# Optimization experiments

Hardware: AMD Instinct MI355X
Metric: run time of the kernel (lower is better)

## Reference

```python
import jax, jax.numpy as jnp
import numpy as np

B, C, H, W = 4, 64, 128, 128
O = 64
K, S, P, D = 3, 1, 1, 1
K2 = K * K
Ho = (H + 2 * P - D * (K - 1) - 1) // S + 1
Wo = (W + 2 * P - D * (K - 1) - 1) // S + 1


def setup_inputs() -> dict:
    key = jax.random.key(0)
    k1, k2, k3, k4, k5 = jax.random.split(key, 5)
    x = jax.random.normal(k1, (B, C, H, W), dtype=jnp.float32)
    fan = C * K2
    # offset conv: out_channels = 2*n_offsets*K*K = 18; small init so offsets are ~O(1) px
    offset_w = jax.random.normal(k2, (2 * K2, C, K, K), dtype=jnp.float32) * (0.1 / np.sqrt(fan))
    offset_b = jax.random.normal(k3, (2 * K2,), dtype=jnp.float32) * 0.01
    deform_w = jax.random.normal(k4, (O, C, K, K), dtype=jnp.float32) * (1.0 / np.sqrt(fan))
    deform_b = jax.random.normal(k5, (O,), dtype=jnp.float32) * 0.01
    return {"x": x, "offset_w": offset_w, "offset_b": offset_b,
            "deform_w": deform_w, "deform_b": deform_b}


def _conv2d(x, w, b):
    y = jax.lax.conv_general_dilated(
        x, w, window_strides=(S, S), padding=[(P, P), (P, P)],
        rhs_dilation=(D, D), dimension_numbers=("NCHW", "OIHW", "NCHW"))
    return y + b[None, :, None, None]


def _gather(flat, iy, ix, h, w):
    # flat: [B, C, H*W]; iy/ix: [B, K2, Ho, Wo] int32
    valid = (iy >= 0) & (iy < h) & (ix >= 0) & (ix < w)
    idx = jnp.clip(iy, 0, h - 1) * w + jnp.clip(ix, 0, w - 1)
    b = flat.shape[0]
    v = jax.vmap(lambda f, i: f[:, i])(flat, idx.reshape(b, -1))  # [B, C, K2*Ho*Wo]
    v = v.reshape(b, flat.shape[1], *idx.shape[1:])               # [B, C, K2, Ho, Wo]
    return v * valid[:, None].astype(flat.dtype)


def _deform_conv(x, offset, w, b):
    # offset: [B, 2*K2, Ho, Wo] laid out as (dy, dx) pairs per kernel tap (torchvision order)
    off = offset.reshape(B, K2, 2, Ho, Wo)
    dy, dx = off[:, :, 0], off[:, :, 1]                           # [B, K2, Ho, Wo]
    ky = (jnp.arange(K2) // K * D).astype(jnp.float32)
    kx = (jnp.arange(K2) % K * D).astype(jnp.float32)
    base_y = (jnp.arange(Ho) * S - P).astype(jnp.float32)
    base_x = (jnp.arange(Wo) * S - P).astype(jnp.float32)
    py = dy + base_y[None, None, :, None] + ky[None, :, None, None]
    px = dx + base_x[None, None, None, :] + kx[None, :, None, None]

    y0 = jnp.floor(py); x0 = jnp.floor(px)
    wy = py - y0; wx = px - x0
    y0i = y0.astype(jnp.int32); x0i = x0.astype(jnp.int32)
    flat = x.reshape(B, C, H * W)
    w00 = ((1 - wy) * (1 - wx))[:, None]
    w01 = ((1 - wy) * wx)[:, None]
    w10 = (wy * (1 - wx))[:, None]
    w11 = (wy * wx)[:, None]
    sampled = (_gather(flat, y0i, x0i, H, W) * w00
               + _gather(flat, y0i, x0i + 1, H, W) * w01
               + _gather(flat, y0i + 1, x0i, H, W) * w10
               + _gather(flat, y0i + 1, x0i + 1, H, W) * w11)  # [B, C, K2, Ho, Wo]
    out = jnp.einsum("bckhw,ock->bohw", sampled, w.reshape(O, C, K2))
    return out + b[None, :, None, None]


def reference(x, offset_w, offset_b, deform_w, deform_b):
    offset = _conv2d(x, offset_w, offset_b)
    return _deform_conv(x, offset, deform_w, deform_b)
```

## Files before the change

### kernel.cpp

```cpp
#include <hip/hip_runtime.h>

#define BB 4
#define CC 64
#define HH 128
#define WW 128
#define OO 64
#define HWs (HH*WW)
#define R9 9
#define XW 20

typedef _Float16 f16;
typedef _Float16 f16x8 __attribute__((ext_vector_type(8)));
typedef _Float16 f16x2 __attribute__((ext_vector_type(2)));
typedef float f32x4 __attribute__((ext_vector_type(4)));

__device__ __forceinline__ size_t xt_idx(int b, int y, int x) {
    return (((size_t)b * HH + y) * WW + x) * CC;
}

__global__ __launch_bounds__(256) void prep_all(const float* __restrict__ x,
                                                const float* __restrict__ offw,
                                                const float* __restrict__ dw,
                                                f16* __restrict__ xt,
                                                f16* __restrict__ wA_off,
                                                f16* __restrict__ wA_def) {
    const int bid = blockIdx.x;
    const int tid = threadIdx.x;
    if (bid < 512) {
        const int b = bid >> 7, y = bid & 127;
        const int px = tid & 127, half = tid >> 7;
        const float* src = x + (size_t)b * CC * HWs + (size_t)half * 32 * HWs + y * WW + px;
        f16* dst = xt + xt_idx(b, y, px) + half * 32;
        #pragma unroll
        for (int cg = 0; cg < 4; ++cg) {
            f16x8 v;
            #pragma unroll
            for (int j = 0; j < 8; ++j)
                v[j] = (f16)src[(size_t)(cg * 8 + j) * HWs];
            *(f16x8*)(dst + cg * 8) = v;
        }
    } else {
        const int t = (bid - 512) * 256 + tid;
        const int l = t & 63;
        const int idx = t >> 6;
        f16x8 v;
        if (idx < 36) {
            const int mt = idx & 1, ks = idx >> 1;
            const int o = mt * 16 + (l & 15);
            const int tap = ks >> 1, ky = tap / 3, kx = tap % 3;
            #pragma unroll
            for (int i = 0; i < 8; ++i) {
                const int c = (ks & 1) * 32 + (l >> 4) * 8 + i;
                v[i] = (o < 18) ? (f16)offw[((o * CC + c) * 3 + ky) * 3 + kx] : (f16)0.f;
            }
            *(f16x8*)(wA_off + (size_t)(idx * 64 + l) * 8) = v;
        } else if (idx < 108) {
            const int id2 = idx - 36;
            const int mt = id2 & 3, ks = (id2 >> 2) & 1, tap = id2 >> 3;
            const int o = mt * 16 + (l & 15);
            #pragma unroll
            for (int i = 0; i < 8; ++i) {
                const int c = ks * 32 + (l >> 4) * 8 + i;
                v[i] = (f16)dw[(size_t)(o * CC + c) * 9 + tap];
            }
            *(f16x8*)(wA_def + (size_t)(id2 * 64 + l) * 8) = v;
        }
    }
}

__device__ __forceinline__ f16x8 combine4(f16x8 p00, f16x8 p01, f16x8 p10, f16x8 p11,
                                          f16 h00, f16 h01, f16 h10, f16 h11) {
    const f16x8 W00 = {h00,h00,h00,h00,h00,h00,h00,h00};
    const f16x8 W01 = {h01,h01,h01,h01,h01,h01,h01,h01};
    const f16x8 W10 = {h10,h10,h10,h10,h10,h10,h10,h10};
    const f16x8 W11 = {h11,h11,h11,h11,h11,h11,h11,h11};
    return p00 * W00 + p01 * W01 + p10 * W10 + p11 * W11;
}

__global__ __launch_bounds__(256, 4) void deform_mfma(
    const f16* __restrict__ xt,
    const f16* __restrict__ wA_off,
    const float* __restrict__ offb,
    const f16* __restrict__ wA_def,
    const float* __restrict__ dbias,
    float* __restrict__ out)
{
    __shared__ __align__(16) char win[R9 * XW * 8 * 16];
    __shared__ float offs[18][64];

    const int tid = threadIdx.x;
    const int bid0 = blockIdx.x;
    const int bid = (bid0 & 7) * 128 + (bid0 >> 3);
    const int b  = bid >> 8;
    const int rg = (bid >> 3) & 31;
    const int pg = bid & 7;
    const int r0 = rg * 4, px0 = pg * 16;

    const int ri = tid >> 6, l = tid & 63;
    const int pxs = l & 15, cg = l >> 4;
    const int row = r0 + ri;
    const int gpx = px0 + pxs;
    const int slot = ri * 16 + pxs;

    #pragma unroll
    for (int it = 0; it < 6; ++it) {
        const int i = tid + it * 256;
        if (i < R9 * XW * 8) {
            const int s = i / (XW * 8), rem = i - s * (XW * 8);
            const int xw = rem >> 3, ch8 = rem & 7;
            const int gy = r0 - 2 + s, gx = px0 - 2 + xw;
            f16x8 v = {};
            if (gy >= 0 && gy < HH && gx >= 0 && gx < WW)
                v = *(const f16x8*)(xt + xt_idx(b, gy, gx) + ch8 * 8);
            *(f16x8*)(win + ((s * XW + xw) * 8 + (ch8 ^ ((xw + s) & 7))) * 16) = v;
        }
    }
    __syncthreads();

    {
        f32x4 oa0 = {0,0,0,0}, oa1 = {0,0,0,0};
        #pragma unroll
        for (int ks = 0; ks < 18; ++ks) {
            const int tap = ks >> 1, chalf = ks & 1;
            const int ky = tap / 3, kx = tap - ky * 3;
            const int s = ri + 1 + ky;
            const int xw = pxs + 1 + kx;
            const int ch8 = chalf * 4 + cg;
            const f16x8 bf = *(const f16x8*)(win + ((s * XW + xw) * 8 + (ch8 ^ ((xw + s) & 7))) * 16);
            const f16x8 a0 = *(const f16x8*)(wA_off + (size_t)((ks * 2 + 0) * 64 + l) * 8);
            const f16x8 a1 = *(const f16x8*)(wA_off + (size_t)((ks * 2 + 1) * 64 + l) * 8);
            oa0 = __builtin_amdgcn_mfma_f32_16x16x32_f16(a0, bf, oa0, 0, 0, 0);
            oa1 = __builtin_amdgcn_mfma_f32_16x16x32_f16(a1, bf, oa1, 0, 0, 0);
        }
        #pragma unroll
        for (int reg = 0; reg < 4; ++reg) {
            const int c0 = cg * 4 + reg;
            offs[c0][slot] = oa0[reg] + offb[c0];
            const int c1 = c0 + 16;
            if (c1 < 18) offs[c1][slot] = oa1[reg] + offb[c1];
        }
    }
    __syncthreads();

    int o00[9], o01[9], o10[9], o11[9];
    f16x2 hA[9], hB[9];
    unsigned okm = 0;
    #pragma unroll
    for (int t = 0; t < 9; ++t) {
        const int ky = t / 3, kx = t - ky * 3;
        const float dy = offs[2 * t][slot], dx = offs[2 * t + 1][slot];
        const float py  = (float)(row - 1 + ky) + dy;
        const float pxf = (float)(gpx - 1 + kx) + dx;
        const float y0f = floorf(py), x0f = floorf(pxf);
        const float wy = py - y0f, wx = pxf - x0f;
        const int y0 = (int)y0f, x0 = (int)x0f;
        const int y1 = y0 + 1, x1 = x0 + 1;
        const bool vy0 = (y0 >= 0) & (y0 < HH), vy1 = (y1 >= 0) & (y1 < HH);
        const bool vx0 = (x0 >= 0) & (x0 < WW), vx1 = (x1 >= 0) & (x1 < WW);
        hA[t][0] = (f16)((1.f - wy) * (1.f - wx) * (float)(vy0 & vx0));
        hA[t][1] = (f16)((1.f - wy) * wx         * (float)(vy0 & vx1));
        hB[t][0] = (f16)(wy * (1.f - wx)         * (float)(vy1 & vx0));
        hB[t][1] = (f16)(wy * wx                 * (float)(vy1 & vx1));
        const int cy0 = min(max(y0, 0), HH - 1), cy1 = min(max(y1, 0), HH - 1);
        const int cx0 = min(max(x0, 0), WW - 1), cx1 = min(max(x1, 0), WW - 1);
        const int s0 = cy0 - (r0 - 2), s1 = cy1 - (r0 - 2);
        const int u0 = cx0 - (px0 - 2), u1 = cx1 - (px0 - 2);
        const int ok = (s0 >= 0) & (s0 < R9) & (s1 >= 0) & (s1 < R9) &
                       (u0 >= 0) & (u0 < XW) & (u1 >= 0) & (u1 < XW);
        if (__all(ok)) okm |= (1u << t);
        const int s0c = min(max(s0, 0), R9 - 1), s1c = min(max(s1, 0), R9 - 1);
        const int u0c = min(max(u0, 0), XW - 1), u1c = min(max(u1, 0), XW - 1);
        o00[t] = ((s0c * XW + u0c) * 8 + (cg ^ ((u0c + s0c) & 7))) * 16;
        o01[t] = ((s0c * XW + u1c) * 8 + (cg ^ ((u1c + s0c) & 7))) * 16;
        o10[t] = ((s1c * XW + u0c) * 8 + (cg ^ ((u0c + s1c) & 7))) * 16;
        o11[t] = ((s1c * XW + u1c) * 8 + (cg ^ ((u1c + s1c) & 7))) * 16;
    }

    f32x4 acc0 = {0,0,0,0}, acc1 = {0,0,0,0}, acc2 = {0,0,0,0}, acc3 = {0,0,0,0};
    const f16* wbase = wA_def + (size_t)l * 8;

    if (okm == 0x1FFu) {
        #pragma unroll
        for (int j = 0; j < 18; ++j) {
            const int t = j >> 1, fl = (j & 1) << 6;
            const f16x8 p00 = *(const f16x8*)(win + (o00[t] ^ fl));
            const f16x8 p01 = *(const f16x8*)(win + (o01[t] ^ fl));
            const f16x8 p10 = *(const f16x8*)(win + (o10[t] ^ fl));
            const f16x8 p11 = *(const f16x8*)(win + (o11[t] ^ fl));
            const f16x8 bf = combine4(p00, p01, p10, p11,
                                      hA[t][0], hA[t][1], hB[t][0], hB[t][1]);
            const f16* wa = wbase + (size_t)j * 2048;
            acc0 = __builtin_amdgcn_mfma_f32_16x16x32_f16(*(const f16x8*)(wa + 0 * 512), bf, acc0, 0, 0, 0);
            acc1 = __builtin_amdgcn_mfma_f32_16x16x32_f16(*(const f16x8*)(wa + 1 * 512), bf, acc1, 0, 0, 0);
            acc2 = __builtin_amdgcn_mfma_f32_16x16x32_f16(*(const f16x8*)(wa + 2 * 512), bf, acc2, 0, 0, 0);
            acc3 = __builtin_amdgcn_mfma_f32_16x16x32_f16(*(const f16x8*)(wa + 3 * 512), bf, acc3, 0, 0, 0);
        }
    } else {
        #pragma unroll
        for (int t = 0; t < 9; ++t) {
            #pragma unroll
            for (int cpass = 0; cpass < 2; ++cpass) {
                const int flip = cpass << 6;
                f16x8 bf;
                if ((okm >> t) & 1) {
                    const f16x8 p00 = *(const f16x8*)(win + (o00[t] ^ flip));
                    const f16x8 p01 = *(const f16x8*)(win + (o01[t] ^ flip));
                    const f16x8 p10 = *(const f16x8*)(win + (o10[t] ^ flip));
                    const f16x8 p11 = *(const f16x8*)(win + (o11[t] ^ flip));
                    bf = combine4(p00, p01, p10, p11,
                                  hA[t][0], hA[t][1], hB[t][0], hB[t][1]);
                } else {
                    const int ky = t / 3, kx = t - ky * 3;
                    const float dy = offs[2 * t][slot], dx = offs[2 * t + 1][slot];
                    const float py  = (float)(row - 1 + ky) + dy;
                    const float pxf = (float)(gpx - 1 + kx) + dx;
                    const int y0 = (int)floorf(py), x0 = (int)floorf(pxf);
                    const int cy0 = min(max(y0, 0), HH - 1), cy1 = min(max(y0 + 1, 0), HH - 1);
                    const int cx0 = min(max(x0, 0), WW - 1), cx1 = min(max(x0 + 1, 0), WW - 1);
                    const int ch8 = cpass * 4 + cg;
                    const f16x8 p00 = *(const f16x8*)(xt + xt_idx(b, cy0, cx0) + ch8 * 8);
                    const f16x8 p01 = *(const f16x8*)(xt + xt_idx(b, cy0, cx1) + ch8 * 8);
                    const f16x8 p10 = *(const f16x8*)(xt + xt_idx(b, cy1, cx0) + ch8 * 8);
                    const f16x8 p11 = *(const f16x8*)(xt + xt_idx(b, cy1, cx1) + ch8 * 8);
                    bf = combine4(p00, p01, p10, p11,
                                  hA[t][0], hA[t][1], hB[t][0], hB[t][1]);
                }
                const f16* wa = wbase + (size_t)(t * 2 + cpass) * 2048;
                acc0 = __builtin_amdgcn_mfma_f32_16x16x32_f16(*(const f16x8*)(wa + 0 * 512), bf, acc0, 0, 0, 0);
                acc1 = __builtin_amdgcn_mfma_f32_16x16x32_f16(*(const f16x8*)(wa + 1 * 512), bf, acc1, 0, 0, 0);
                acc2 = __builtin_amdgcn_mfma_f32_16x16x32_f16(*(const f16x8*)(wa + 2 * 512), bf, acc2, 0, 0, 0);
                acc3 = __builtin_amdgcn_mfma_f32_16x16x32_f16(*(const f16x8*)(wa + 3 * 512), bf, acc3, 0, 0, 0);
            }
        }
    }

    #pragma unroll
    for (int mt = 0; mt < 4; ++mt) {
        const f32x4 a = (mt == 0) ? acc0 : (mt == 1) ? acc1 : (mt == 2) ? acc2 : acc3;
        #pragma unroll
        for (int reg = 0; reg < 4; ++reg) {
            const int o = mt * 16 + cg * 4 + reg;
            out[(((size_t)b * OO + o) * HH + row) * WW + gpx] = a[reg] + dbias[o];
        }
    }
}

extern "C" void kernel_launch(void* const* d_in, const int* in_sizes, int n_in,
                              void* d_out, int out_size, void* d_ws, size_t ws_size,
                              hipStream_t stream) {
    const float* x     = (const float*)d_in[0];
    const float* offw  = (const float*)d_in[1];
    const float* offb  = (const float*)d_in[2];
    const float* dw    = (const float*)d_in[3];
    const float* dbias = (const float*)d_in[4];
    float* out = (float*)d_out;

    const size_t XT_BYTES    = (size_t)BB * HH * WW * CC * sizeof(f16);
    const size_t WAOFF_BYTES = 36 * 64 * 8 * sizeof(f16);

    f16* xt     = (f16*)d_ws;
    f16* wa_off = (f16*)((char*)d_ws + XT_BYTES);
    f16* wa_def = (f16*)((char*)d_ws + XT_BYTES + WAOFF_BYTES);
    (void)ws_size; (void)in_sizes; (void)n_in; (void)out_size;

    prep_all<<<512 + 27, 256, 0, stream>>>(x, offw, dw, xt, wa_off, wa_def);
    deform_mfma<<<1024, 256, 0, stream>>>(xt, wa_off, offb, wa_def, dbias, out);
}
```

Measured before the change: 37.58 us.

## Switch to 32x32x16 MFMA with 32-pixel tiles and wider halo window

Replaces the 16x16x32 MFMA tiles with 32x32x16 MFMA for both the offset conv and the deform conv. Each block now covers 4 rows x 32 pixels (halo window widened to 36 columns), so the grid is halved and the weight-fragment layout in prep is rearranged to match. The intent is to cut weight-fragment loads and MFMA issue count per output and to reuse the shared-memory window across more pixels. In exchange the kernel uses more shared memory and accumulator registers (launch bounds lowered to 3 blocks per SIMD), has fewer blocks in flight, and the offset MFMA wastes most of its 32 rows on padding.

```diff
diff --git a/kernel.cpp b/kernel.cpp
--- a/kernel.cpp
+++ b/kernel.cpp
@@ -7,12 +7,12 @@
 #define OO 64
 #define HWs (HH*WW)
 #define R9 9
-#define XW 20
+#define XW 36
 
 typedef _Float16 f16;
 typedef _Float16 f16x8 __attribute__((ext_vector_type(8)));
 typedef _Float16 f16x2 __attribute__((ext_vector_type(2)));
-typedef float f32x4 __attribute__((ext_vector_type(4)));
+typedef float f32x16 __attribute__((ext_vector_type(16)));
 
 __device__ __forceinline__ size_t xt_idx(int b, int y, int x) {
     return (((size_t)b * HH + y) * WW + x) * CC;
@@ -45,23 +45,24 @@
         const int idx = t >> 6;
         f16x8 v;
         if (idx < 36) {
-            const int mt = idx & 1, ks = idx >> 1;
-            const int o = mt * 16 + (l & 15);
-            const int tap = ks >> 1, ky = tap / 3, kx = tap % 3;
+            const int ks = idx;
+            const int m = l & 31;
             #pragma unroll
             for (int i = 0; i < 8; ++i) {
-                const int c = (ks & 1) * 32 + (l >> 4) * 8 + i;
-                v[i] = (o < 18) ? (f16)offw[((o * CC + c) * 3 + ky) * 3 + kx] : (f16)0.f;
+                const int k = ks * 16 + (l >> 5) * 8 + i;
+                const int tap = k >> 6, c = k & 63;
+                const int ky = tap / 3, kx = tap % 3;
+                v[i] = (m < 18) ? (f16)offw[((m * CC + c) * 3 + ky) * 3 + kx] : (f16)0.f;
             }
             *(f16x8*)(wA_off + (size_t)(idx * 64 + l) * 8) = v;
         } else if (idx < 108) {
             const int id2 = idx - 36;
-            const int mt = id2 & 3, ks = (id2 >> 2) & 1, tap = id2 >> 3;
-            const int o = mt * 16 + (l & 15);
+            const int ot = id2 & 1, ks2 = (id2 >> 1) & 3, tap = id2 >> 3;
+            const int m = ot * 32 + (l & 31);
             #pragma unroll
             for (int i = 0; i < 8; ++i) {
-                const int c = ks * 32 + (l >> 4) * 8 + i;
-                v[i] = (f16)dw[(size_t)(o * CC + c) * 9 + tap];
+                const int c = ks2 * 16 + (l >> 5) * 8 + i;
+                v[i] = (f16)dw[(size_t)(m * CC + c) * 9 + tap];
             }
             *(f16x8*)(wA_def + (size_t)(id2 * 64 + l) * 8) = v;
         }
@@ -77,7 +78,7 @@
     return p00 * W00 + p01 * W01 + p10 * W10 + p11 * W11;
 }
 
-__global__ __launch_bounds__(256, 4) void deform_mfma(
+__global__ __launch_bounds__(256, 3) void deform_mfma(
     const f16* __restrict__ xt,
     const f16* __restrict__ wA_off,
     const float* __restrict__ offb,
@@ -86,24 +87,24 @@
     float* __restrict__ out)
 {
     __shared__ __align__(16) char win[R9 * XW * 8 * 16];
-    __shared__ float offs[18][64];
+    __shared__ float offs[18][128];
 
     const int tid = threadIdx.x;
     const int bid0 = blockIdx.x;
-    const int bid = (bid0 & 7) * 128 + (bid0 >> 3);
-    const int b  = bid >> 8;
-    const int rg = (bid >> 3) & 31;
-    const int pg = bid & 7;
-    const int r0 = rg * 4, px0 = pg * 16;
+    const int bid = (bid0 & 7) * 64 + (bid0 >> 3);
+    const int b  = bid >> 7;
+    const int rg = (bid >> 2) & 31;
+    const int pg = bid & 3;
+    const int r0 = rg * 4, px0 = pg * 32;
 
     const int ri = tid >> 6, l = tid & 63;
-    const int pxs = l & 15, cg = l >> 4;
+    const int n  = l & 31, kh = l >> 5;
     const int row = r0 + ri;
-    const int gpx = px0 + pxs;
-    const int slot = ri * 16 + pxs;
+    const int gpx = px0 + n;
+    const int slot = ri * 32 + n;
 
     #pragma unroll
-    for (int it = 0; it < 6; ++it) {
+    for (int it = 0; it < 11; ++it) {
         const int i = tid + it * 256;
         if (i < R9 * XW * 8) {
             const int s = i / (XW * 8), rem = i - s * (XW * 8);
@@ -118,26 +119,22 @@
     __syncthreads();
 
     {
-        f32x4 oa0 = {0,0,0,0}, oa1 = {0,0,0,0};
-        #pragma unroll
-        for (int ks = 0; ks < 18; ++ks) {
-            const int tap = ks >> 1, chalf = ks & 1;
+        f32x16 oa = {0,0,0,0,0,0,0,0,0,0,0,0,0,0,0,0};
+        #pragma unroll
+        for (int ks = 0; ks < 36; ++ks) {
+            const int tap = ks >> 2;
             const int ky = tap / 3, kx = tap - ky * 3;
             const int s = ri + 1 + ky;
-            const int xw = pxs + 1 + kx;
-            const int ch8 = chalf * 4 + cg;
+            const int xw = n + 1 + kx;
+            const int ch8 = (ks & 3) * 2 + kh;
             const f16x8 bf = *(const f16x8*)(win + ((s * XW + xw) * 8 + (ch8 ^ ((xw + s) & 7))) * 16);
-            const f16x8 a0 = *(const f16x8*)(wA_off + (size_t)((ks * 2 + 0) * 64 + l) * 8);
-            const f16x8 a1 = *(const f16x8*)(wA_off + (size_t)((ks * 2 + 1) * 64 + l) * 8);
-            oa0 = __builtin_amdgcn_mfma_f32_16x16x32_f16(a0, bf, oa0, 0, 0, 0);
-            oa1 = __builtin_amdgcn_mfma_f32_16x16x32_f16(a1, bf, oa1, 0, 0, 0);
-        }
-        #pragma unroll
-        for (int reg = 0; reg < 4; ++reg) {
-            const int c0 = cg * 4 + reg;
-            offs[c0][slot] = oa0[reg] + offb[c0];
-            const int c1 = c0 + 16;
-            if (c1 < 18) offs[c1][slot] = oa1[reg] + offb[c1];
+            const f16x8 a = *(const f16x8*)(wA_off + (size_t)(ks * 64 + l) * 8);
+            oa = __builtin_amdgcn_mfma_f32_32x32x16_f16(a, bf, oa, 0, 0, 0);
+        }
+        #pragma unroll
+        for (int reg = 0; reg < 16; ++reg) {
+            const int ch = (reg & 3) + 8 * (reg >> 2) + 4 * kh;
+            if (ch < 18) offs[ch][slot] = oa[reg] + offb[ch];
         }
     }
     __syncthreads();
@@ -170,43 +167,42 @@
         if (__all(ok)) okm |= (1u << t);
         const int s0c = min(max(s0, 0), R9 - 1), s1c = min(max(s1, 0), R9 - 1);
         const int u0c = min(max(u0, 0), XW - 1), u1c = min(max(u1, 0), XW - 1);
-        o00[t] = ((s0c * XW + u0c) * 8 + (cg ^ ((u0c + s0c) & 7))) * 16;
-        o01[t] = ((s0c * XW + u1c) * 8 + (cg ^ ((u1c + s0c) & 7))) * 16;
-        o10[t] = ((s1c * XW + u0c) * 8 + (cg ^ ((u0c + s1c) & 7))) * 16;
-        o11[t] = ((s1c * XW + u1c) * 8 + (cg ^ ((u1c + s1c) & 7))) * 16;
-    }
-
-    f32x4 acc0 = {0,0,0,0}, acc1 = {0,0,0,0}, acc2 = {0,0,0,0}, acc3 = {0,0,0,0};
+        o00[t] = ((s0c * XW + u0c) * 8 + (kh ^ ((u0c + s0c) & 7))) * 16;
+        o01[t] = ((s0c * XW + u1c) * 8 + (kh ^ ((u1c + s0c) & 7))) * 16;
+        o10[t] = ((s1c * XW + u0c) * 8 + (kh ^ ((u0c + s1c) & 7))) * 16;
+        o11[t] = ((s1c * XW + u1c) * 8 + (kh ^ ((u1c + s1c) & 7))) * 16;
+    }
+
+    f32x16 acc0 = {0,0,0,0,0,0,0,0,0,0,0,0,0,0,0,0};
+    f32x16 acc1 = {0,0,0,0,0,0,0,0,0,0,0,0,0,0,0,0};
     const f16* wbase = wA_def + (size_t)l * 8;
 
     if (okm == 0x1FFu) {
         #pragma unroll
-        for (int j = 0; j < 18; ++j) {
-            const int t = j >> 1, fl = (j & 1) << 6;
+        for (int j = 0; j < 36; ++j) {
+            const int t = j >> 2, fl = (j & 3) << 5;
             const f16x8 p00 = *(const f16x8*)(win + (o00[t] ^ fl));
             const f16x8 p01 = *(const f16x8*)(win + (o01[t] ^ fl));
             const f16x8 p10 = *(const f16x8*)(win + (o10[t] ^ fl));
             const f16x8 p11 = *(const f16x8*)(win + (o11[t] ^ fl));
             const f16x8 bf = combine4(p00, p01, p10, p11,
                                       hA[t][0], hA[t][1], hB[t][0], hB[t][1]);
-            const f16* wa = wbase + (size_t)j * 2048;
-            acc0 = __builtin_amdgcn_mfma_f32_16x16x32_f16(*(const f16x8*)(wa + 0 * 512), bf, acc0, 0, 0, 0);
-            acc1 = __builtin_amdgcn_mfma_f32_16x16x32_f16(*(const f16x8*)(wa + 1 * 512), bf, acc1, 0, 0, 0);
-            acc2 = __builtin_amdgcn_mfma_f32_16x16x32_f16(*(const f16x8*)(wa + 2 * 512), bf, acc2, 0, 0, 0);
-            acc3 = __builtin_amdgcn_mfma_f32_16x16x32_f16(*(const f16x8*)(wa + 3 * 512), bf, acc3, 0, 0, 0);
+            const f16* wa = wbase + (size_t)j * 1024;
+            acc0 = __builtin_amdgcn_mfma_f32_32x32x16_f16(*(const f16x8*)(wa + 0 * 512), bf, acc0, 0, 0, 0);
+            acc1 = __builtin_amdgcn_mfma_f32_32x32x16_f16(*(const f16x8*)(wa + 1 * 512), bf, acc1, 0, 0, 0);
         }
     } else {
         #pragma unroll
         for (int t = 0; t < 9; ++t) {
             #pragma unroll
-            for (int cpass = 0; cpass < 2; ++cpass) {
-                const int flip = cpass << 6;
+            for (int ks2 = 0; ks2 < 4; ++ks2) {
+                const int fl = ks2 << 5;
                 f16x8 bf;
                 if ((okm >> t) & 1) {
-                    const f16x8 p00 = *(const f16x8*)(win + (o00[t] ^ flip));
-                    const f16x8 p01 = *(const f16x8*)(win + (o01[t] ^ flip));
-                    const f16x8 p10 = *(const f16x8*)(win + (o10[t] ^ flip));
-                    const f16x8 p11 = *(const f16x8*)(win + (o11[t] ^ flip));
+                    const f16x8 p00 = *(const f16x8*)(win + (o00[t] ^ fl));
+                    const f16x8 p01 = *(const f16x8*)(win + (o01[t] ^ fl));
+                    const f16x8 p10 = *(const f16x8*)(win + (o10[t] ^ fl));
+                    const f16x8 p11 = *(const f16x8*)(win + (o11[t] ^ fl));
                     bf = combine4(p00, p01, p10, p11,
                                   hA[t][0], hA[t][1], hB[t][0], hB[t][1]);
                 } else {
@@ -217,31 +213,26 @@
                     const int y0 = (int)floorf(py), x0 = (int)floorf(pxf);
                     const int cy0 = min(max(y0, 0), HH - 1), cy1 = min(max(y0 + 1, 0), HH - 1);
                     const int cx0 = min(max(x0, 0), WW - 1), cx1 = min(max(x0 + 1, 0), WW - 1);
-                    const int ch8 = cpass * 4 + cg;
-                    const f16x8 p00 = *(const f16x8*)(xt + xt_idx(b, cy0, cx0) + ch8 * 8);
-                    const f16x8 p01 = *(const f16x8*)(xt + xt_idx(b, cy0, cx1) + ch8 * 8);
-                    const f16x8 p10 = *(const f16x8*)(xt + xt_idx(b, cy1, cx0) + ch8 * 8);
-                    const f16x8 p11 = *(const f16x8*)(xt + xt_idx(b, cy1, cx1) + ch8 * 8);
+                    const int cb = ks2 * 16 + kh * 8;
+                    const f16x8 p00 = *(const f16x8*)(xt + xt_idx(b, cy0, cx0) + cb);
+                    const f16x8 p01 = *(const f16x8*)(xt + xt_idx(b, cy0, cx1) + cb);
+                    const f16x8 p10 = *(const f16x8*)(xt + xt_idx(b, cy1, cx0) + cb);
+                    const f16x8 p11 = *(const f16x8*)(xt + xt_idx(b, cy1, cx1) + cb);
                     bf = combine4(p00, p01, p10, p11,
                                   hA[t][0], hA[t][1], hB[t][0], hB[t][1]);
                 }
-                const f16* wa = wbase + (size_t)(t * 2 + cpass) * 2048;
-                acc0 = __builtin_amdgcn_mfma_f32_16x16x32_f16(*(const f16x8*)(wa + 0 * 512), bf, acc0, 0, 0, 0);
-                acc1 = __builtin_amdgcn_mfma_f32_16x16x32_f16(*(const f16x8*)(wa + 1 * 512), bf, acc1, 0, 0, 0);
-                acc2 = __builtin_amdgcn_mfma_f32_16x16x32_f16(*(const f16x8*)(wa + 2 * 512), bf, acc2, 0, 0, 0);
-                acc3 = __builtin_amdgcn_mfma_f32_16x16x32_f16(*(const f16x8*)(wa + 3 * 512), bf, acc3, 0, 0, 0);
+                const f16* wa = wbase + (size_t)(t * 4 + ks2) * 1024;
+                acc0 = __builtin_amdgcn_mfma_f32_32x32x16_f16(*(const f16x8*)(wa + 0 * 512), bf, acc0, 0, 0, 0);
+                acc1 = __builtin_amdgcn_mfma_f32_32x32x16_f16(*(const f16x8*)(wa + 1 * 512), bf, acc1, 0, 0, 0);
             }
         }
     }
 
     #pragma unroll
-    for (int mt = 0; mt < 4; ++mt) {
-        const f32x4 a = (mt == 0) ? acc0 : (mt == 1) ? acc1 : (mt == 2) ? acc2 : acc3;
-        #pragma unroll
-        for (int reg = 0; reg < 4; ++reg) {
-            const int o = mt * 16 + cg * 4 + reg;
-            out[(((size_t)b * OO + o) * HH + row) * WW + gpx] = a[reg] + dbias[o];
-        }
+    for (int reg = 0; reg < 16; ++reg) {
+        const int oc = (reg & 3) + 8 * (reg >> 2) + 4 * kh;
+        out[(((size_t)b * OO + oc) * HH + row) * WW + gpx]        = acc0[reg] + dbias[oc];
+        out[(((size_t)b * OO + oc + 32) * HH + row) * WW + gpx]   = acc1[reg] + dbias[oc + 32];
     }
 }
 
@@ -264,5 +255,5 @@
     (void)ws_size; (void)in_sizes; (void)n_in; (void)out_size;
 
     prep_all<<<512 + 27, 256, 0, stream>>>(x, offw, dw, xt, wa_off, wa_def);
-    deform_mfma<<<1024, 256, 0, stream>>>(xt, wa_off, offb, wa_def, dbias, out);
-}
+    deform_mfma<<<512, 256, 0, stream>>>(xt, wa_off, offb, wa_def, dbias, out);
+}
```

After: 45.08 us. 1.2x slower.
